# Optimization experiments

Hardware: AMD Instinct MI355X
Metric: run time of the kernel (lower is better)

## Reference

```python
import jax, jax.numpy as jnp
import numpy as np

B, S, D, H = 4, 1024, 1024, 16
DK = D // H  # f_out = 64


def setup_inputs() -> dict:
    key = jax.random.key(0)
    ks = jax.random.split(key, 20)
    sc = 0.02
    inp = {
        "q": jax.random.normal(ks[0], (B, S, D), jnp.float32),
        "k": jax.random.normal(ks[1], (B, S, D), jnp.float32),
        "v": jax.random.normal(ks[2], (B, S, D), jnp.float32),
        "mask": jnp.ones((B * H, S), jnp.int32),
        # q_lin / k_lin / v_lin: Linear(num_hiddens=D, num_q=D)
        "Wq": jax.random.normal(ks[3], (D, D), jnp.float32) * sc,
        "bq": jnp.zeros((D,), jnp.float32),
        "Wk": jax.random.normal(ks[4], (D, D), jnp.float32) * sc,
        "bk": jnp.zeros((D,), jnp.float32),
        "Wv": jax.random.normal(ks[5], (D, D), jnp.float32) * sc,
        "bv": jnp.zeros((D,), jnp.float32),
        # per-head FeedForward (Linear f_out->f_out + ReLU; dropout is a no-op in eval)
        "Wqf": jax.random.normal(ks[6], (DK, DK), jnp.float32) * sc,
        "bqf": jnp.zeros((DK,), jnp.float32),
        "Wkf": jax.random.normal(ks[7], (DK, DK), jnp.float32) * sc,
        "bkf": jnp.zeros((DK,), jnp.float32),
        "Wvf": jax.random.normal(ks[8], (DK, DK), jnp.float32) * sc,
        "bvf": jnp.zeros((DK,), jnp.float32),
        # out: Linear(f_out, f_out), applied per head before recombining
        "Wo": jax.random.normal(ks[9], (DK, DK), jnp.float32) * sc,
        "bo": jnp.zeros((DK,), jnp.float32),
    }
    return inp


def reference(q, k, v, mask, Wq, bq, Wk, bk, Wv, bv,
              Wqf, bqf, Wkf, bkf, Wvf, bvf, Wo, bo):
    def lin(x, W, b):
        return jnp.einsum("...i,oi->...o", x, W) + b

    def split_heads(x):  # (B,S,D) -> (B*H,S,DK)
        return x.reshape(B, S, H, DK).transpose(0, 2, 1, 3).reshape(B * H, S, DK)

    # projections + head split + per-head FeedForward (Linear -> ReLU)
    Q = jax.nn.relu(lin(split_heads(lin(q, Wq, bq)), Wqf, bqf))
    K = jax.nn.relu(lin(split_heads(lin(k, Wk, bk)), Wkf, bkf))
    V = jax.nn.relu(lin(split_heads(lin(v, Wv, bv)), Wvf, bvf))

    # scaled dot-product attention with padding mask (dropout = identity, eval)
    scores = jnp.einsum("bqd,bkd->bqk", Q, K) / np.sqrt(DK).astype(np.float32)
    scores = jnp.where(mask[:, None, :] == 0, -10000.0, scores)
    attn = jax.nn.softmax(scores, axis=-1)
    out = jnp.einsum("bqk,bkd->bqd", attn, V)  # (B*H,S,DK)

    out = lin(out, Wo, bo)  # per-head output projection (DK -> DK)
    # transpose_output: (B*H,S,DK) -> (B,S,H*DK)
    out = out.reshape(B, H, S, DK).transpose(0, 2, 1, 3).reshape(B, S, H * DK)
    return out
```

## Files before the change

kernel.cpp:

```cpp
#include <hip/hip_runtime.h>
#include <stdint.h>

#define MM 4096
#define SS 1024
#define DD 1024
#define HH 16
#define DKK 64

typedef __bf16 bf16x8 __attribute__((ext_vector_type(8)));
typedef __bf16 bf16x4 __attribute__((ext_vector_type(4)));
typedef float  f32x4  __attribute__((ext_vector_type(4)));

#define LOG2E 1.44269504088896340736f

__device__ __forceinline__ void gload_lds16(const void* g, void* l) {
  __builtin_amdgcn_global_load_lds(
      (__attribute__((address_space(1))) void*)g,
      (__attribute__((address_space(3))) void*)l, 16, 0, 0);
}

#define LSW(row, ch) ((row) * 64 + ((((ch) ^ ((row) & 7)) << 3)))

__global__ __launch_bounds__(256) void prep(
    const float* __restrict__ q, const float* __restrict__ k,
    const float* __restrict__ v,
    const float* __restrict__ Wq, const float* __restrict__ bq,
    const float* __restrict__ Wk, const float* __restrict__ bk,
    const float* __restrict__ Wv, const float* __restrict__ bv,
    const float* __restrict__ Wqf, const float* __restrict__ bqf,
    const float* __restrict__ Wkf, const float* __restrict__ bkf,
    const float* __restrict__ Wvf, const float* __restrict__ bvf,
    __bf16* __restrict__ X3, __bf16* __restrict__ Wc3,
    float* __restrict__ bc3) {
  int blk = blockIdx.x;
  if (blk < 6144) {
    int z = blk >> 11;
    int bx = blk & 2047;
    const float* src = (z == 0) ? q : ((z == 1) ? k : v);
    size_t i = ((size_t)bx * 256 + threadIdx.x) * 8;
    float4 a = *(const float4*)(src + i);
    float4 b = *(const float4*)(src + i + 4);
    bf16x8 r;
    r[0] = (__bf16)a.x; r[1] = (__bf16)a.y; r[2] = (__bf16)a.z; r[3] = (__bf16)a.w;
    r[4] = (__bf16)b.x; r[5] = (__bf16)b.y; r[6] = (__bf16)b.z; r[7] = (__bf16)b.w;
    *(bf16x8*)(X3 + (size_t)z * MM * DD + i) = r;
  } else {
    int t = blk - 6144;
    int z = t >> 8;
    int rem = t & 255;
    int h = rem >> 4, ic = (rem >> 2) & 3, jc = rem & 3;
    const float* W   = (z == 0) ? Wq  : ((z == 1) ? Wk  : Wv);
    const float* bs  = (z == 0) ? bq  : ((z == 1) ? bk  : bv);
    const float* Wf  = (z == 0) ? Wqf : ((z == 1) ? Wkf : Wvf);
    const float* bf_ = (z == 0) ? bqf : ((z == 1) ? bkf : bvf);
    int i = ic * 256 + threadIdx.x;
    const float* wfb = Wf + jc * 16 * DKK;

    float acc[16];
#pragma unroll
    for (int jj = 0; jj < 16; ++jj) acc[jj] = 0.f;
#pragma unroll 4
    for (int d = 0; d < 64; ++d) {
      float wv = W[(size_t)(h * DKK + d) * DD + i];
#pragma unroll
      for (int jj = 0; jj < 16; ++jj)
        acc[jj] = fmaf(wfb[jj * DKK + d], wv, acc[jj]);
    }
#pragma unroll
    for (int jj = 0; jj < 16; ++jj)
      Wc3[(size_t)z * DD * DD + (size_t)(h * DKK + jc * 16 + jj) * DD + i] =
          (__bf16)acc[jj];

    if (ic == 0 && jc == 0 && threadIdx.x < 64) {
      int j = threadIdx.x;
      float bb = bf_[j];
      for (int d = 0; d < 64; ++d) bb += Wf[j * DKK + d] * bs[h * DKK + d];
      bc3[z * DD + h * DKK + j] = bb;
    }
  }
}

__global__ __launch_bounds__(256) void gemm3(const __bf16* __restrict__ X3,
                                             const __bf16* __restrict__ Wc3,
                                             const float* __restrict__ bc3,
                                             __bf16* __restrict__ QKV) {
  __shared__ __bf16 As[128 * 64];
  __shared__ __bf16 Bs[128 * 64];
  const int z = blockIdx.z;
  const __bf16* A  = X3  + (size_t)z * MM * DD;
  const __bf16* Bt = Wc3 + (size_t)z * DD * DD;
  const float* bias = bc3 + z * DD;
  __bf16* C = QKV + (size_t)z * MM * DD;

  const int tid = threadIdx.x;
  const int wave = tid >> 6, lane = tid & 63;
  const int l15 = lane & 15, l4 = lane >> 4;
  const int bm = blockIdx.x * 128;
  const int bn = blockIdx.y * 128;
  const int wr = (wave >> 1) * 64;
  const int wc = (wave & 1) * 64;

  f32x4 acc[4][4] = {};

  const int srow = wave * 8 + (lane >> 3);
  const int scol = (lane & 7) * 8;

  for (int kt = 0; kt < DD; kt += 64) {
    __syncthreads();
#pragma unroll
    for (int j = 0; j < 4; ++j) {
      int row = j * 32 + srow;
      gload_lds16(A  + (size_t)(bm + row) * DD + kt + scol, As + j * 2048 + wave * 512);
      gload_lds16(Bt + (size_t)(bn + row) * DD + kt + scol, Bs + j * 2048 + wave * 512);
    }
    asm volatile("s_waitcnt vmcnt(0)" ::: "memory");
    __syncthreads();
#pragma unroll
    for (int ks = 0; ks < 2; ++ks) {
      bf16x8 af[4], bfr[4];
#pragma unroll
      for (int mi = 0; mi < 4; ++mi)
        af[mi] = *(const bf16x8*)(As + (wr + mi * 16 + l15) * 64 + ks * 32 + l4 * 8);
#pragma unroll
      for (int ni = 0; ni < 4; ++ni)
        bfr[ni] = *(const bf16x8*)(Bs + (wc + ni * 16 + l15) * 64 + ks * 32 + l4 * 8);
#pragma unroll
      for (int mi = 0; mi < 4; ++mi)
#pragma unroll
        for (int ni = 0; ni < 4; ++ni)
          acc[mi][ni] = __builtin_amdgcn_mfma_f32_16x16x32_bf16(af[mi], bfr[ni], acc[mi][ni], 0, 0, 0);
    }
  }

#pragma unroll
  for (int ni = 0; ni < 4; ++ni) {
    int n = bn + wc + ni * 16 + l15;
    float bb = bias[n];
#pragma unroll
    for (int mi = 0; mi < 4; ++mi) {
      if (z != 2) {
#pragma unroll
        for (int r = 0; r < 4; ++r) {
          int m = bm + wr + mi * 16 + l4 * 4 + r;
          float vv = acc[mi][ni][r] + bb;
          vv = vv > 0.f ? vv : 0.f;
          C[(size_t)m * DD + n] = (__bf16)vv;
        }
      } else {
        int m0 = bm + wr + mi * 16 + l4 * 4;
        int b = m0 >> 10, s0 = m0 & 1023;
        int h = n >> 6, dk = n & 63;
        bf16x4 pk;
#pragma unroll
        for (int r = 0; r < 4; ++r) {
          float vv = acc[mi][ni][r] + bb;
          vv = vv > 0.f ? vv : 0.f;
          pk[r] = (__bf16)vv;
        }
        *(bf16x4*)(C + ((size_t)(b * HH + h) * DKK + dk) * SS + s0) = pk;
      }
    }
  }
}

__global__ __launch_bounds__(512) void attn_kernel(
    const __bf16* __restrict__ Q,
    const __bf16* __restrict__ K,
    const __bf16* __restrict__ Vt,
    const int* __restrict__ mask,
    const float* __restrict__ Wo,
    const float* __restrict__ bo,
    float* __restrict__ out)
{
  __shared__ __bf16 Qs[128 * 64];
  __shared__ __bf16 Ks[2][64 * 64];
  __shared__ __bf16 Vs[2][64 * 64];
  __shared__ __bf16 Pw[8][16 * 64];
  __shared__ __bf16 Wos[64 * 64];

  const int tid = threadIdx.x;
  const int wave = tid >> 6, lane = tid & 63;
  const int l15 = lane & 15, l4 = lane >> 4;

  const int lin = blockIdx.x;
  const int swz = (lin & 7) * 64 + (lin >> 3);
  const int qt = swz & 7;
  const int bh = swz >> 3;
  const int b = bh >> 4, h = bh & 15;

  const __bf16* Qbase = Q + ((size_t)b * SS + qt * 128) * DD + h * 64;
  const __bf16* Kbase = K + (size_t)b * SS * DD + h * 64;
  const __bf16* Vbase = Vt + (size_t)bh * DKK * SS;

  for (int t = tid; t < 64 * 64; t += 512) {
    int row = t >> 6, col = t & 63;
    Wos[row * 64 + ((((col >> 3) ^ (row & 7)) << 3) | (col & 7))] = (__bf16)Wo[t];
  }

  const int lr8 = lane >> 3;
  const int scol = (((lane & 7) ^ lr8) * 8);
  const int krow = wave * 8 + lr8;

#pragma unroll
  for (int j = 0; j < 2; ++j)
    gload_lds16(Qbase + (size_t)(wave * 16 + j * 8 + lr8) * DD + scol,
                Qs + wave * 1024 + j * 512);
  gload_lds16(Kbase + (size_t)krow * DD + scol, Ks[0] + wave * 512);
  gload_lds16(Vbase + (size_t)krow * SS + scol, Vs[0] + wave * 512);
  asm volatile("s_waitcnt vmcnt(0)" ::: "memory");
  __syncthreads();

  f32x4 o_acc[4] = {};
  float mrow[4], lrow[4];
#pragma unroll
  for (int r = 0; r < 4; ++r) { mrow[r] = -1e30f; lrow[r] = 0.f; }

  const float SCL = 0.125f * LOG2E;

  for (int kt = 0; kt < SS / 64; ++kt) {
    const int cur = kt & 1;
    if (kt < SS / 64 - 1) {
      gload_lds16(Kbase + (size_t)((kt + 1) * 64 + krow) * DD + scol,
                  Ks[cur ^ 1] + wave * 512);
      gload_lds16(Vbase + (size_t)krow * SS + (kt + 1) * 64 + scol,
                  Vs[cur ^ 1] + wave * 512);
    }

    f32x4 sc[4] = {};
#pragma unroll
    for (int ks = 0; ks < 2; ++ks) {
      bf16x8 aq = *(const bf16x8*)(Qs + LSW(wave * 16 + l15, ks * 4 + l4));
#pragma unroll
      for (int ni = 0; ni < 4; ++ni) {
        bf16x8 kf = *(const bf16x8*)(Ks[cur] + LSW(ni * 16 + l15, ks * 4 + l4));
        sc[ni] = __builtin_amdgcn_mfma_f32_16x16x32_bf16(aq, kf, sc[ni], 0, 0, 0);
      }
    }
#pragma unroll
    for (int ni = 0; ni < 4; ++ni) {
      int key = kt * 64 + ni * 16 + l15;
      int mv = mask[bh * SS + key];
#pragma unroll
      for (int r = 0; r < 4; ++r) {
        float s = sc[ni][r] * SCL;
        sc[ni][r] = (mv == 0) ? (-10000.f * LOG2E) : s;
      }
    }
    float alpha[4];
#pragma unroll
    for (int r = 0; r < 4; ++r) {
      float v = fmaxf(fmaxf(sc[0][r], sc[1][r]), fmaxf(sc[2][r], sc[3][r]));
      v = fmaxf(v, __shfl_xor(v, 1));
      v = fmaxf(v, __shfl_xor(v, 2));
      v = fmaxf(v, __shfl_xor(v, 4));
      v = fmaxf(v, __shfl_xor(v, 8));
      float mnew = fmaxf(mrow[r], v);
      alpha[r] = __builtin_exp2f(mrow[r] - mnew);
      mrow[r] = mnew;
      float s = 0.f;
#pragma unroll
      for (int ni = 0; ni < 4; ++ni) {
        float p = __builtin_exp2f(sc[ni][r] - mnew);
        sc[ni][r] = p;
        s += p;
      }
      s += __shfl_xor(s, 1); s += __shfl_xor(s, 2);
      s += __shfl_xor(s, 4); s += __shfl_xor(s, 8);
      lrow[r] = lrow[r] * alpha[r] + s;
    }
#pragma unroll
    for (int ni = 0; ni < 4; ++ni)
#pragma unroll
      for (int r = 0; r < 4; ++r) {
        int row = l4 * 4 + r;
        int ch = 2 * ni + (l15 >> 3);
        Pw[wave][row * 64 + (((ch ^ (row & 7)) << 3) | (l15 & 7))] = (__bf16)sc[ni][r];
      }
    asm volatile("" ::: "memory");
#pragma unroll
    for (int ni = 0; ni < 4; ++ni)
#pragma unroll
      for (int r = 0; r < 4; ++r) o_acc[ni][r] *= alpha[r];
#pragma unroll
    for (int ks = 0; ks < 2; ++ks) {
      bf16x8 ap = *(const bf16x8*)(&Pw[wave][LSW(l15, ks * 4 + l4)]);
#pragma unroll
      for (int ni = 0; ni < 4; ++ni) {
        bf16x8 vf = *(const bf16x8*)(Vs[cur] + LSW(ni * 16 + l15, ks * 4 + l4));
        o_acc[ni] = __builtin_amdgcn_mfma_f32_16x16x32_bf16(ap, vf, o_acc[ni], 0, 0, 0);
      }
    }
    asm volatile("s_waitcnt vmcnt(0)" ::: "memory");
    __syncthreads();
  }

#pragma unroll
  for (int ni = 0; ni < 4; ++ni)
#pragma unroll
    for (int r = 0; r < 4; ++r) {
      int row = l4 * 4 + r;
      int ch = 2 * ni + (l15 >> 3);
      Pw[wave][row * 64 + (((ch ^ (row & 7)) << 3) | (l15 & 7))] =
          (__bf16)(o_acc[ni][r] / lrow[r]);
    }
  asm volatile("" ::: "memory");
  f32x4 facc[4] = {};
#pragma unroll
  for (int ks = 0; ks < 2; ++ks) {
    bf16x8 ao = *(const bf16x8*)(&Pw[wave][LSW(l15, ks * 4 + l4)]);
#pragma unroll
    for (int ni = 0; ni < 4; ++ni) {
      bf16x8 wf = *(const bf16x8*)(Wos + LSW(ni * 16 + l15, ks * 4 + l4));
      facc[ni] = __builtin_amdgcn_mfma_f32_16x16x32_bf16(ao, wf, facc[ni], 0, 0, 0);
    }
  }
#pragma unroll
  for (int ni = 0; ni < 4; ++ni) {
    int j = ni * 16 + l15;
    float bb = bo[j];
#pragma unroll
    for (int r = 0; r < 4; ++r) {
      int qrow = qt * 128 + wave * 16 + l4 * 4 + r;
      out[((size_t)b * SS + qrow) * DD + h * 64 + j] = facc[ni][r] + bb;
    }
  }
}

extern "C" void kernel_launch(void* const* d_in, const int* in_sizes, int n_in,
                              void* d_out, int out_size, void* d_ws, size_t ws_size,
                              hipStream_t stream) {
  const float* q   = (const float*)d_in[0];
  const float* k   = (const float*)d_in[1];
  const float* v   = (const float*)d_in[2];
  const int*   mask= (const int*)d_in[3];
  const float* Wq  = (const float*)d_in[4];
  const float* bq  = (const float*)d_in[5];
  const float* Wk  = (const float*)d_in[6];
  const float* bk  = (const float*)d_in[7];
  const float* Wv  = (const float*)d_in[8];
  const float* bv  = (const float*)d_in[9];
  const float* Wqf = (const float*)d_in[10];
  const float* bqf = (const float*)d_in[11];
  const float* Wkf = (const float*)d_in[12];
  const float* bkf = (const float*)d_in[13];
  const float* Wvf = (const float*)d_in[14];
  const float* bvf = (const float*)d_in[15];
  const float* Wo  = (const float*)d_in[16];
  const float* bo  = (const float*)d_in[17];
  float* out = (float*)d_out;

  char* p = (char*)d_ws;
  __bf16* X3  = (__bf16*)p; p += (size_t)3 * MM * DD * 2;
  __bf16* Wc3 = (__bf16*)p; p += (size_t)3 * DD * DD * 2;
  __bf16* QKV = (__bf16*)p; p += (size_t)3 * MM * DD * 2;
  float*  bc3 = (float*)p;  p += (size_t)3 * DD * 4;
  if ((size_t)(p - (char*)d_ws) > ws_size) return;

  prep<<<6912, 256, 0, stream>>>(q, k, v, Wq, bq, Wk, bk, Wv, bv,
                                 Wqf, bqf, Wkf, bkf, Wvf, bvf, X3, Wc3, bc3);
  gemm3<<<dim3(32, 8, 3), 256, 0, stream>>>(X3, Wc3, bc3, QKV);
  attn_kernel<<<512, 512, 0, stream>>>(
      QKV, QKV + (size_t)MM * DD, QKV + (size_t)2 * MM * DD, mask, Wo, bo, out);
}
```

Measured before the change: 245.5 us.

## Transpose attention MFMA operands so each lane owns one query row

Swaps the A/B operands of every MFMA so each lane holds one query row and four consecutive keys or columns. Row max and sum then need only two cross-lane shuffles instead of four per row, and P and the output can be written with vector stores. Also hoists the Q fragment loads out of the key loop, precomputes the mask as a float bias in shared memory applied with fminf, skips the accumulator rescale when no lane's max changed, and writes output as float4. The cost is extra shared memory for the bias table and a wave-uniform branch per iteration.

```diff
diff --git a/kernel.cpp b/kernel.cpp
--- a/kernel.cpp
+++ b/kernel.cpp
@@ -177,6 +177,7 @@
   __shared__ __bf16 Vs[2][64 * 64];
   __shared__ __bf16 Pw[8][16 * 64];
   __shared__ __bf16 Wos[64 * 64];
+  __shared__ float  Biasf[1024];
 
   const int tid = threadIdx.x;
   const int wave = tid >> 6, lane = tid & 63;
@@ -196,6 +197,8 @@
     int row = t >> 6, col = t & 63;
     Wos[row * 64 + ((((col >> 3) ^ (row & 7)) << 3) | (col & 7))] = (__bf16)Wo[t];
   }
+  for (int t = tid; t < 1024; t += 512)
+    Biasf[t] = mask[bh * SS + t] ? 1e30f : (-10000.f * LOG2E);
 
   const int lr8 = lane >> 3;
   const int scol = (((lane & 7) ^ lr8) * 8);
@@ -210,12 +213,18 @@
   asm volatile("s_waitcnt vmcnt(0)" ::: "memory");
   __syncthreads();
 
+  bf16x8 aq[2];
+#pragma unroll
+  for (int ks = 0; ks < 2; ++ks)
+    aq[ks] = *(const bf16x8*)(Qs + LSW(wave * 16 + l15, ks * 4 + l4));
+
   f32x4 o_acc[4] = {};
-  float mrow[4], lrow[4];
-#pragma unroll
-  for (int r = 0; r < 4; ++r) { mrow[r] = -1e30f; lrow[r] = 0.f; }
-
+  float mrow = -1e30f, lrow = 0.f;
   const float SCL = 0.125f * LOG2E;
+
+  const int pwoff = l15 * 64;
+  const int pwch0 = (l4 >> 1);
+  const int pwin  = (l4 & 1) << 2;
 
   for (int kt = 0; kt < SS / 64; ++kt) {
     const int cur = kt & 1;
@@ -229,80 +238,79 @@
     f32x4 sc[4] = {};
 #pragma unroll
     for (int ks = 0; ks < 2; ++ks) {
-      bf16x8 aq = *(const bf16x8*)(Qs + LSW(wave * 16 + l15, ks * 4 + l4));
 #pragma unroll
       for (int ni = 0; ni < 4; ++ni) {
         bf16x8 kf = *(const bf16x8*)(Ks[cur] + LSW(ni * 16 + l15, ks * 4 + l4));
-        sc[ni] = __builtin_amdgcn_mfma_f32_16x16x32_bf16(aq, kf, sc[ni], 0, 0, 0);
+        sc[ni] = __builtin_amdgcn_mfma_f32_16x16x32_bf16(kf, aq[ks], sc[ni], 0, 0, 0);
       }
     }
 #pragma unroll
     for (int ni = 0; ni < 4; ++ni) {
-      int key = kt * 64 + ni * 16 + l15;
-      int mv = mask[bh * SS + key];
+      float4 bb = *(const float4*)(Biasf + kt * 64 + ni * 16 + (l4 << 2));
+      sc[ni][0] = fminf(sc[ni][0] * SCL, bb.x);
+      sc[ni][1] = fminf(sc[ni][1] * SCL, bb.y);
+      sc[ni][2] = fminf(sc[ni][2] * SCL, bb.z);
+      sc[ni][3] = fminf(sc[ni][3] * SCL, bb.w);
+    }
+    float m = fmaxf(fmaxf(sc[0][0], sc[0][1]), fmaxf(sc[0][2], sc[0][3]));
+#pragma unroll
+    for (int ni = 1; ni < 4; ++ni)
+      m = fmaxf(m, fmaxf(fmaxf(sc[ni][0], sc[ni][1]), fmaxf(sc[ni][2], sc[ni][3])));
+    m = fmaxf(m, __shfl_xor(m, 16));
+    m = fmaxf(m, __shfl_xor(m, 32));
+    float mnew = fmaxf(mrow, m);
+    float alpha = __builtin_exp2f(mrow - mnew);
+    mrow = mnew;
+    float s = 0.f;
+#pragma unroll
+    for (int ni = 0; ni < 4; ++ni)
 #pragma unroll
       for (int r = 0; r < 4; ++r) {
-        float s = sc[ni][r] * SCL;
-        sc[ni][r] = (mv == 0) ? (-10000.f * LOG2E) : s;
-      }
-    }
-    float alpha[4];
-#pragma unroll
-    for (int r = 0; r < 4; ++r) {
-      float v = fmaxf(fmaxf(sc[0][r], sc[1][r]), fmaxf(sc[2][r], sc[3][r]));
-      v = fmaxf(v, __shfl_xor(v, 1));
-      v = fmaxf(v, __shfl_xor(v, 2));
-      v = fmaxf(v, __shfl_xor(v, 4));
-      v = fmaxf(v, __shfl_xor(v, 8));
-      float mnew = fmaxf(mrow[r], v);
-      alpha[r] = __builtin_exp2f(mrow[r] - mnew);
-      mrow[r] = mnew;
-      float s = 0.f;
-#pragma unroll
-      for (int ni = 0; ni < 4; ++ni) {
         float p = __builtin_exp2f(sc[ni][r] - mnew);
         sc[ni][r] = p;
         s += p;
       }
-      s += __shfl_xor(s, 1); s += __shfl_xor(s, 2);
-      s += __shfl_xor(s, 4); s += __shfl_xor(s, 8);
-      lrow[r] = lrow[r] * alpha[r] + s;
-    }
-#pragma unroll
-    for (int ni = 0; ni < 4; ++ni)
-#pragma unroll
-      for (int r = 0; r < 4; ++r) {
-        int row = l4 * 4 + r;
-        int ch = 2 * ni + (l15 >> 3);
-        Pw[wave][row * 64 + (((ch ^ (row & 7)) << 3) | (l15 & 7))] = (__bf16)sc[ni][r];
-      }
+    s += __shfl_xor(s, 16);
+    s += __shfl_xor(s, 32);
+    lrow = lrow * alpha + s;
+
+#pragma unroll
+    for (int ni = 0; ni < 4; ++ni) {
+      bf16x4 w;
+      w[0] = (__bf16)sc[ni][0]; w[1] = (__bf16)sc[ni][1];
+      w[2] = (__bf16)sc[ni][2]; w[3] = (__bf16)sc[ni][3];
+      int ch = (2 * ni + pwch0) ^ (l15 & 7);
+      *(bf16x4*)(&Pw[wave][pwoff + (ch << 3) + pwin]) = w;
+    }
     asm volatile("" ::: "memory");
-#pragma unroll
-    for (int ni = 0; ni < 4; ++ni)
-#pragma unroll
-      for (int r = 0; r < 4; ++r) o_acc[ni][r] *= alpha[r];
+    if (!__all(alpha == 1.0f)) {
+#pragma unroll
+      for (int ni = 0; ni < 4; ++ni)
+#pragma unroll
+        for (int r = 0; r < 4; ++r) o_acc[ni][r] *= alpha;
+    }
 #pragma unroll
     for (int ks = 0; ks < 2; ++ks) {
       bf16x8 ap = *(const bf16x8*)(&Pw[wave][LSW(l15, ks * 4 + l4)]);
 #pragma unroll
       for (int ni = 0; ni < 4; ++ni) {
         bf16x8 vf = *(const bf16x8*)(Vs[cur] + LSW(ni * 16 + l15, ks * 4 + l4));
-        o_acc[ni] = __builtin_amdgcn_mfma_f32_16x16x32_bf16(ap, vf, o_acc[ni], 0, 0, 0);
+        o_acc[ni] = __builtin_amdgcn_mfma_f32_16x16x32_bf16(vf, ap, o_acc[ni], 0, 0, 0);
       }
     }
     asm volatile("s_waitcnt vmcnt(0)" ::: "memory");
     __syncthreads();
   }
 
-#pragma unroll
-  for (int ni = 0; ni < 4; ++ni)
-#pragma unroll
-    for (int r = 0; r < 4; ++r) {
-      int row = l4 * 4 + r;
-      int ch = 2 * ni + (l15 >> 3);
-      Pw[wave][row * 64 + (((ch ^ (row & 7)) << 3) | (l15 & 7))] =
-          (__bf16)(o_acc[ni][r] / lrow[r]);
-    }
+  float rinv = 1.0f / lrow;
+#pragma unroll
+  for (int ni = 0; ni < 4; ++ni) {
+    bf16x4 w;
+    w[0] = (__bf16)(o_acc[ni][0] * rinv); w[1] = (__bf16)(o_acc[ni][1] * rinv);
+    w[2] = (__bf16)(o_acc[ni][2] * rinv); w[3] = (__bf16)(o_acc[ni][3] * rinv);
+    int ch = (2 * ni + pwch0) ^ (l15 & 7);
+    *(bf16x4*)(&Pw[wave][pwoff + (ch << 3) + pwin]) = w;
+  }
   asm volatile("" ::: "memory");
   f32x4 facc[4] = {};
 #pragma unroll
@@ -311,18 +319,19 @@
 #pragma unroll
     for (int ni = 0; ni < 4; ++ni) {
       bf16x8 wf = *(const bf16x8*)(Wos + LSW(ni * 16 + l15, ks * 4 + l4));
-      facc[ni] = __builtin_amdgcn_mfma_f32_16x16x32_bf16(ao, wf, facc[ni], 0, 0, 0);
-    }
-  }
+      facc[ni] = __builtin_amdgcn_mfma_f32_16x16x32_bf16(wf, ao, facc[ni], 0, 0, 0);
+    }
+  }
+  const int qrow = qt * 128 + wave * 16 + l15;
+  float* orow = out + ((size_t)b * SS + qrow) * DD + h * 64;
 #pragma unroll
   for (int ni = 0; ni < 4; ++ni) {
-    int j = ni * 16 + l15;
-    float bb = bo[j];
-#pragma unroll
-    for (int r = 0; r < 4; ++r) {
-      int qrow = qt * 128 + wave * 16 + l4 * 4 + r;
-      out[((size_t)b * SS + qrow) * DD + h * 64 + j] = facc[ni][r] + bb;
-    }
+    int j0 = ni * 16 + (l4 << 2);
+    float4 bov = *(const float4*)(bo + j0);
+    float4 ov;
+    ov.x = facc[ni][0] + bov.x; ov.y = facc[ni][1] + bov.y;
+    ov.z = facc[ni][2] + bov.z; ov.w = facc[ni][3] + bov.w;
+    *(float4*)(orow + j0) = ov;
   }
 }
 
```

New measurement: 234.3 us. -4.6%, faster.
